# Optimization experiments

Measured on AMD Instinct MI355X. Metric: run time of the kernel, lower is better.

The kernel has to match this reference:

```python
import jax, jax.numpy as jnp
import numpy as np

NF = 32
B, H, W = 4, 256, 256


def conv(x, w, b, pad):
    y = jax.lax.conv_general_dilated(x, w, (1, 1), [(pad, pad), (pad, pad)],
                                     dimension_numbers=('NCHW', 'OIHW', 'NCHW'))
    return y + b[None, :, None, None]


def maxpool(x):  # kernel 3, stride 2, pad 1 (pad with -inf like torch)
    return jax.lax.reduce_window(x, -jnp.inf, jax.lax.max,
                                 (1, 1, 3, 3), (1, 1, 2, 2),
                                 [(0, 0), (0, 0), (1, 1), (1, 1)])


def up2(x):  # bilinear x2, align_corners=False (half-pixel) == jax.image default
    b, c, h, w = x.shape
    return jax.image.resize(x, (b, c, 2 * h, 2 * w), 'bilinear')


def norm_gates(g1, g2, g3):
    s = jnp.abs(g1) + jnp.abs(g2) + jnp.abs(g3)
    s = jnp.where(s == 0, 1e-6, s)
    m = (s >= 1).astype(g1.dtype)
    return tuple((1 - m) * g + m * (g / s) for g in (g1, g2, g3))


def propagate(x, g1, g2, g3, horizontal, reverse):
    """GateRecurrent2dnoind: sequential gated scan along one spatial axis.
    h[t] = (1 - g1 - g2 - g3) * x[t] + g1*h[t-1](i-1) + g2*h[t-1](i) + g3*h[t-1](i+1)
    with zero boundary for out-of-range neighbors."""
    if not horizontal:
        x, g1, g2, g3 = (jnp.swapaxes(t, 2, 3) for t in (x, g1, g2, g3))
    if reverse:
        x, g1, g2, g3 = (t[..., ::-1] for t in (x, g1, g2, g3))
    seqs = tuple(jnp.moveaxis(t, 3, 0) for t in (x, g1, g2, g3))  # [W,B,C,H]

    def step(h, inp):
        xt, a1, a2, a3 = inp
        z = jnp.zeros_like(h[..., :1])
        h_up = jnp.concatenate([z, h[..., :-1]], axis=-1)   # neighbor i-1
        h_dn = jnp.concatenate([h[..., 1:], z], axis=-1)    # neighbor i+1
        hn = (1 - a1 - a2 - a3) * xt + a1 * h_up + a2 * h + a3 * h_dn
        return hn, hn

    h0 = jnp.zeros(x.shape[:3], x.dtype)
    _, ys = jax.lax.scan(step, h0, seqs)
    out = jnp.moveaxis(ys, 0, 3)
    if reverse:
        out = out[..., ::-1]
    if not horizontal:
        out = jnp.swapaxes(out, 2, 3)
    return out


def spn_forward(x, rgb, mw, mb, c1w, c1b, c2w, c2b, c3w, c3b, c4w, c4b,
                d0w, d0b, d2w, d2b, d4w, d4b, d6w, d6b, d7w, d7b, pw, pb):
    nf = NF
    X = conv(x, mw, mb, 1)
    # VGG encoder
    f1 = conv(rgb, c1w, c1b, 1)
    p = maxpool(jax.nn.relu(f1))
    f2 = conv(p, c2w, c2b, 1)
    p = maxpool(jax.nn.relu(f2))
    f3 = conv(p, c3w, c3b, 1)
    p3 = maxpool(jax.nn.relu(f3))
    f4 = conv(p3, c4w, c4b, 1)
    # Decoder
    o = conv(f4, d0w, d0b, 0)
    o = jax.nn.elu(conv(up2(o), d2w, d2b, 1)) + f3
    o = jax.nn.elu(conv(up2(o), d4w, d4b, 1)) + f2
    o = jax.nn.elu(conv(up2(o), d6w, d6b, 1)) + f1
    guide = conv(o, d7w, d7b, 1)  # [B, 12*nf, H, W]
    G = [guide[:, i * nf:(i + 1) * nf] for i in range(12)]
    dirs = [(True, False), (True, True), (False, False), (False, True)]
    outs = []
    for k, (hor, rev) in enumerate(dirs):
        g1, g2, g3 = norm_gates(G[3 * k], G[3 * k + 1], G[3 * k + 2])
        outs.append(propagate(X, g1, g2, g3, hor, rev))
    out = jnp.maximum(jnp.maximum(outs[0], outs[1]), jnp.maximum(outs[2], outs[3]))
    return conv(out, pw, pb, 1)


def setup_inputs() -> dict:
    key = jax.random.key(0)
    ks = jax.random.split(key, 32)
    nf = NF

    def p(k, shape):
        return jax.random.normal(k, shape, dtype=jnp.float32) * 0.1

    inp = {
        'x': jax.random.normal(ks[0], (B, 3, H, W), dtype=jnp.float32),
        'rgb': jax.random.normal(ks[1], (B, 3, H, W), dtype=jnp.float32),
        'mw': p(ks[2], (nf, 3, 3, 3)), 'mb': p(ks[3], (nf,)),
        'c1w': p(ks[4], (nf, 3, 3, 3)), 'c1b': p(ks[5], (nf,)),
        'c2w': p(ks[6], (nf * 2, nf, 3, 3)), 'c2b': p(ks[7], (nf * 2,)),
        'c3w': p(ks[8], (nf * 4, nf * 2, 3, 3)), 'c3b': p(ks[9], (nf * 4,)),
        'c4w': p(ks[10], (nf * 8, nf * 4, 3, 3)), 'c4b': p(ks[11], (nf * 8,)),
        'd0w': p(ks[12], (nf * 4, nf * 8, 1, 1)), 'd0b': p(ks[13], (nf * 4,)),
        'd2w': p(ks[14], (nf * 4, nf * 4, 3, 3)), 'd2b': p(ks[15], (nf * 4,)),
        'd4w': p(ks[16], (nf * 2, nf * 4, 3, 3)), 'd4b': p(ks[17], (nf * 2,)),
        'd6w': p(ks[18], (nf, nf * 2, 3, 3)), 'd6b': p(ks[19], (nf,)),
        'd7w': p(ks[20], (nf * 12, nf, 3, 3)), 'd7b': p(ks[21], (nf * 12,)),
        'pw': p(ks[22], (3, nf, 3, 3)), 'pb': p(ks[23], (3,)),
    }
    return inp


def reference(x, rgb, mw, mb, c1w, c1b, c2w, c2b, c3w, c3b, c4w, c4b,
              d0w, d0b, d2w, d2b, d4w, d4b, d6w, d6b, d7w, d7b, pw, pb):
    return spn_forward(x, rgb, mw, mb, c1w, c1b, c2w, c2b, c3w, c3b, c4w, c4b,
                       d0w, d0b, d2w, d2b, d4w, d4b, d6w, d6b, d7w, d7b, pw, pb)
```

## Files before the change

### kernel.cpp

```cpp
#include <hip/hip_runtime.h>
#include <cstddef>
#include <cstdint>

#define DEVINL __device__ __forceinline__

typedef __attribute__((ext_vector_type(8))) _Float16 half8v;
typedef __attribute__((ext_vector_type(4))) _Float16 half4v;
typedef __attribute__((ext_vector_type(16))) float f32x16;

constexpr int cmax(int a, int b) { return a > b ? a : b; }


__global__ __launch_bounds__(256) void k_repack(
    const float* __restrict__ src, float* __restrict__ dst, int Cin, int Cout)
{
  int n = Cout * Cin * 9;
  int e = blockIdx.x * 256 + threadIdx.x;
  if (e >= n) return;
  int co = e / (Cin * 9);
  int r  = e - co * Cin * 9;
  int ci = r / 9;
  int k  = r - ci * 9;
  dst[(ci * 9 + k) * Cout + co] = src[e];
}

__global__ __launch_bounds__(256) void k_packwh(
    const float* __restrict__ src, _Float16* __restrict__ dst, int Cin, int Cout)
{
  int chunks = Cin >> 4;
  int total = Cout * chunks * 144;
  int e = blockIdx.x * 256 + threadIdx.x;
  if (e >= total) return;
  int n  = e / (chunks * 144);
  int r2 = e - n * chunks * 144;
  int cb = r2 / 144;
  int k  = r2 - cb * 144;
  int tap = k >> 4, ci = k & 15;
  float v = src[((size_t)n * Cin + cb * 16 + ci) * 9 + tap];
  dst[((size_t)cb * Cout + n) * 152 + k] = (_Float16)v;
}

template<int NWM, int NACC, int CHUNKS, int MODE, int GATES>
__global__ __launch_bounds__(NWM * 64) void k_convh(
    const float* __restrict__ in, const _Float16* __restrict__ wpk,
    const float* __restrict__ bias, const float* __restrict__ skip,
    void* __restrict__ outv,
    int H, int W, int wCout, int n0, int outC, int oco0)
{
  static_assert(GATES == 0 || NACC == 3, "GATES needs NACC==3");
  constexpr int NTHR = NWM * 64;
  constexpr int ROWS = NWM * 2;
  constexpr int RH = ROWS + 2;
  constexpr int N_BLK = NACC * 32;
  constexpr int MT = NWM * 32;
  constexpr int A_BYTES = RH * 18 * 16 * 2;
  constexpr int B_BYTES = N_BLK * 152 * 2;
  constexpr int MPF = MT + 1;
  constexpr int MPH = 132;
  constexpr int EP_BYTES = GATES ? (96 * MPH * 2) : (N_BLK * MPF * 4);
  constexpr int SMEM = cmax(A_BYTES + B_BYTES, EP_BYTES);

  const int tid = threadIdx.x;
  const int wave = tid >> 6, lane = tid & 63;
  const int wm = wave;
  const int tiles_x = W >> 4;
  const int tx0 = (blockIdx.x % tiles_x) << 4;
  const int ty0 = (blockIdx.x / tiles_x) * ROWS;
  const int b = blockIdx.z;
  const int nb = n0 + blockIdx.y * N_BLK;
  const int ocb = oco0 + blockIdx.y * N_BLK;

  __shared__ __align__(16) char smem[SMEM];
  _Float16* Ah = (_Float16*)smem;
  _Float16* Bh = (_Float16*)(smem + A_BYTES);

  f32x16 acc[NACC] = {};

  const size_t ps = (size_t)H * W;
  const float* inb = in + (size_t)b * (CHUNKS * 16) * ps;

  for (int cb = 0; cb < CHUNKS; ++cb) {
    __syncthreads();
    for (int e = tid; e < RH * 18; e += NTHR) {
      int r = e / 18, c = e - r * 18;
      int gy = ty0 + r - 1, gx = tx0 + c - 1;
      bool ok = (unsigned)gy < (unsigned)H && (unsigned)gx < (unsigned)W;
      const float* src = inb + (size_t)(cb * 16) * ps + (size_t)gy * W + gx;
      half8v v0, v1;
#pragma unroll
      for (int j = 0; j < 8; ++j)
        v0[j] = ok ? (_Float16)src[(size_t)j * ps] : (_Float16)0.f;
#pragma unroll
      for (int j = 0; j < 8; ++j)
        v1[j] = ok ? (_Float16)src[(size_t)(j + 8) * ps] : (_Float16)0.f;
      *(half8v*)&Ah[e * 16] = v0;
      *(half8v*)&Ah[e * 16 + 8] = v1;
    }
    {
      const _Float16* wsrc = wpk + ((size_t)cb * wCout + nb) * 152;
      for (int e = tid; e < N_BLK * 19; e += NTHR)
        *(uint4*)&Bh[e * 8] = *(const uint4*)(wsrc + e * 8);
    }
    __syncthreads();
    const int am = wm * 32 + (lane & 31);
    const int r0 = am >> 4, c0 = am & 15;
    const int kh = lane >> 5;
    const _Float16* Ab = Ah + kh * 8;
    const _Float16* Bb = Bh + kh * 8;
#pragma unroll
    for (int ks = 0; ks < 9; ++ks) {
      const int dy = ks / 3, dx = ks - dy * 3;
      half8v af = *(const half8v*)(Ab + ((r0 + dy) * 18 + (c0 + dx)) * 16);
#pragma unroll
      for (int na = 0; na < NACC; ++na) {
        const int bn = na * 32 + (lane & 31);
        half8v bf = *(const half8v*)(Bb + bn * 152 + ks * 16);
        acc[na] = __builtin_amdgcn_mfma_f32_32x32x16_f16(af, bf, acc[na], 0, 0, 0);
      }
    }
  }

  __syncthreads();

  if (GATES) {
    _Float16* EPH = (_Float16*)smem;
    const int c = lane & 31;
    const float bv0 = bias[nb + c];
    const float bv1 = bias[nb + 32 + c];
    const float bv2 = bias[nb + 64 + c];
#pragma unroll
    for (int i = 0; i < 16; ++i) {
      int m = wm * 32 + (i & 3) + 8 * (i >> 2) + 4 * (lane >> 5);
      float g1 = acc[0][i] + bv0;
      float g2 = acc[GATES ? 1 : 0][i] + bv1;
      float g3 = acc[GATES ? 2 : 0][i] + bv2;
      float s = fabsf(g1) + fabsf(g2) + fabsf(g3);
      if (s >= 1.f) { float r = 1.f / s; g1 *= r; g2 *= r; g3 *= r; }
      EPH[(size_t)(0 * 32 + c) * MPH + m] = (_Float16)g1;
      EPH[(size_t)(1 * 32 + c) * MPH + m] = (_Float16)g2;
      EPH[(size_t)(2 * 32 + c) * MPH + m] = (_Float16)g3;
    }
    __syncthreads();
    _Float16* outh = (_Float16*)outv;
    if (MODE == 2) {
      const int TOT = 96 * 16;
      for (int r = tid; r < TOT; r += NTHR) {
        int gc = r >> 4, x = r & 15;
        const _Float16* ep = EPH + (size_t)gc * MPH + x;
        _Float16 v[8];
#pragma unroll
        for (int y = 0; y < 8; ++y) v[y] = ep[y * 16];
        size_t base = ((size_t)(b * 96 + gc) * W + tx0 + x) * (size_t)H + ty0;
        *(uint4*)(outh + base) = *(const uint4*)v;
      }
    } else {
      const int TOT = 96 * ROWS;
      for (int r = tid; r < TOT; r += NTHR) {
        int gc = r / ROWS, y = r - gc * ROWS;
        const _Float16* ep = EPH + (size_t)gc * MPH + y * 16;
        _Float16 v[16];
#pragma unroll
        for (int x = 0; x < 16; ++x) v[x] = ep[x];
        size_t base = ((size_t)(b * 96 + gc) * H + ty0 + y) * (size_t)W + tx0;
        *(uint4*)(outh + base) = *(const uint4*)v;
        *(uint4*)(outh + base + 8) = *(const uint4*)(v + 8);
      }
    }
  } else {
    float* EP = (float*)smem;
    float bv[NACC];
#pragma unroll
    for (int na = 0; na < NACC; ++na) bv[na] = bias[nb + na * 32 + (lane & 31)];
#pragma unroll
    for (int na = 0; na < NACC; ++na) {
      const int c = na * 32 + (lane & 31);
#pragma unroll
      for (int i = 0; i < 16; ++i) {
        int m = wm * 32 + (i & 3) + 8 * (i >> 2) + 4 * (lane >> 5);
        EP[(size_t)c * MPF + m] = acc[na][i] + bv[na];
      }
    }
    __syncthreads();
    float* out = (float*)outv;
    const int TOT = N_BLK * ROWS;
    for (int r = tid; r < TOT; r += NTHR) {
      int c = r / ROWS, y = r - c * ROWS;
      const float* ep = EP + (size_t)c * MPF + y * 16;
      float v[16];
#pragma unroll
      for (int x = 0; x < 16; ++x) v[x] = ep[x];
      size_t base = (((size_t)b * outC + ocb + c) * H + ty0 + y) * (size_t)W + tx0;
      if (MODE == 1) {
#pragma unroll
        for (int j = 0; j < 4; ++j) {
          float4 sk = *(const float4*)(skip + base + 4 * j);
          float e0 = v[4*j+0] > 0.f ? v[4*j+0] : expm1f(v[4*j+0]);
          float e1 = v[4*j+1] > 0.f ? v[4*j+1] : expm1f(v[4*j+1]);
          float e2 = v[4*j+2] > 0.f ? v[4*j+2] : expm1f(v[4*j+2]);
          float e3 = v[4*j+3] > 0.f ? v[4*j+3] : expm1f(v[4*j+3]);
          v[4*j+0] = e0 + sk.x; v[4*j+1] = e1 + sk.y;
          v[4*j+2] = e2 + sk.z; v[4*j+3] = e3 + sk.w;
        }
      }
#pragma unroll
      for (int j = 0; j < 4; ++j)
        *(float4*)(out + base + 4 * j) = *(const float4*)(v + 4 * j);
    }
  }
}

template<int CI, int CO>
__global__ __launch_bounds__(256) void k_conv3x3f(
    const float* __restrict__ in, const float* __restrict__ wr,
    const float* __restrict__ bias, float* __restrict__ out,
    int Cin, int H, int W, int wstride, int outC)
{
  const int ntx = W >> 4;
  const int tid = threadIdx.x;
  const int tx = tid & 15, ty = tid >> 4;
  const int tx0 = (blockIdx.x % ntx) << 4, ty0 = (blockIdx.x / ntx) << 4;
  const int b = blockIdx.z;

  __shared__ float sh[CI * 324];

  float acc[CO];
#pragma unroll
  for (int co = 0; co < CO; ++co) acc[co] = bias[co];

  const float* inb = in + (size_t)b * Cin * H * W;

  for (int cb = 0; cb < Cin; cb += CI) {
    __syncthreads();
    for (int e = tid; e < CI * 324; e += 256) {
      int ci = e / 324;
      int rr = e - ci * 324;
      int r = rr / 18, c = rr - r * 18;
      int gh = ty0 + r - 1, gw = tx0 + c - 1;
      float v = 0.f;
      if ((unsigned)gh < (unsigned)H && (unsigned)gw < (unsigned)W)
        v = inb[(size_t)(cb + ci) * H * W + (size_t)gh * W + gw];
      sh[e] = v;
    }
    __syncthreads();
#pragma unroll 1
    for (int ci = 0; ci < CI; ++ci) {
      float v[9];
      const float* sp = sh + ci * 324 + ty * 18 + tx;
#pragma unroll
      for (int kh = 0; kh < 3; ++kh)
#pragma unroll
        for (int kw = 0; kw < 3; ++kw)
          v[kh * 3 + kw] = sp[kh * 18 + kw];
      const float* wp = wr + (size_t)((cb + ci) * 9) * wstride;
#pragma unroll
      for (int k = 0; k < 9; ++k)
#pragma unroll
        for (int co = 0; co < CO; ++co)
          acc[co] = fmaf(wp[(size_t)k * wstride + co], v[k], acc[co]);
    }
  }
#pragma unroll
  for (int co = 0; co < CO; ++co)
    out[(((size_t)b * outC + co) * H + ty0 + ty) * W + tx0 + tx] = acc[co];
}

__global__ __launch_bounds__(256) void k_convfin(
    const _Float16* __restrict__ om1, const _Float16* __restrict__ om2,
    const _Float16* __restrict__ omT1, const _Float16* __restrict__ omT2,
    const float* __restrict__ wr, const float* __restrict__ bias,
    float* __restrict__ out)
{
  const int H = 256, W = 256;
  const int tid = threadIdx.x;
  const int tx = tid & 15, ty = tid >> 4;
  const int tx0 = (blockIdx.x & 15) << 4, ty0 = (blockIdx.x >> 4) << 4;
  const int b = blockIdx.z;

  __shared__ float sh[32 * 324];

  for (int e = tid; e < 32 * 324; e += 256) {
    int ci = e / 324, rr = e - ci * 324;
    int r = rr / 18, c = rr - r * 18;
    int gh = ty0 + r - 1, gw = tx0 + c - 1;
    float v = 0.f;
    if ((unsigned)gh < (unsigned)H && (unsigned)gw < (unsigned)W) {
      size_t p = ((size_t)(b * 32 + ci) * H + gh) * W + gw;
      v = fmaxf((float)om1[p], (float)om2[p]);
    }
    sh[ci * 324 + r * 18 + c] = v;
  }
  __syncthreads();
  for (int e = tid; e < 32 * 324; e += 256) {
    int ci = e / 324, rr = e - ci * 324;
    int c = rr / 18, r = rr - c * 18;
    int gh = ty0 + r - 1, gw = tx0 + c - 1;
    if ((unsigned)gh < (unsigned)H && (unsigned)gw < (unsigned)W) {
      size_t p = ((size_t)(b * 32 + ci) * W + gw) * (size_t)H + gh;
      float t = fmaxf((float)omT1[p], (float)omT2[p]);
      int si = ci * 324 + r * 18 + c;
      sh[si] = fmaxf(sh[si], t);
    }
  }
  __syncthreads();

  float acc[3] = {bias[0], bias[1], bias[2]};
#pragma unroll 1
  for (int ci = 0; ci < 32; ++ci) {
    float v[9];
    const float* sp = sh + ci * 324 + ty * 18 + tx;
#pragma unroll
    for (int kh = 0; kh < 3; ++kh)
#pragma unroll
      for (int kw = 0; kw < 3; ++kw)
        v[kh * 3 + kw] = sp[kh * 18 + kw];
    const float* wp = wr + (size_t)(ci * 9) * 3;
#pragma unroll
    for (int k = 0; k < 9; ++k)
#pragma unroll
      for (int co = 0; co < 3; ++co)
        acc[co] = fmaf(wp[(size_t)k * 3 + co], v[k], acc[co]);
  }
#pragma unroll
  for (int co = 0; co < 3; ++co)
    out[(((size_t)b * 3 + co) * H + ty0 + ty) * W + tx0 + tx] = acc[co];
}

__global__ __launch_bounds__(256) void k_conv1x1(
    const float* __restrict__ in, const float* __restrict__ wgt,
    const float* __restrict__ bias, float* __restrict__ out,
    int Cin, int Cout, int H, int W)
{
  int hw = blockIdx.x * 256 + threadIdx.x;
  if (hw >= H * W) return;
  int co = blockIdx.y, b = blockIdx.z;
  const float* ip = in + (size_t)b * Cin * H * W + hw;
  const float* wp = wgt + (size_t)co * Cin;
  float acc = bias[co];
  for (int ci = 0; ci < Cin; ++ci) acc += wp[ci] * ip[(size_t)ci * H * W];
  out[((size_t)b * Cout + co) * H * W + hw] = acc;
}

__global__ __launch_bounds__(256) void k_pool(
    const float* __restrict__ in, float* __restrict__ out, int C, int H, int W)
{
  int Ho = H >> 1, Wo = W >> 1;
  int hw = blockIdx.x * 256 + threadIdx.x;
  if (hw >= Ho * Wo) return;
  int ow = hw % Wo, oh = hw / Wo;
  int c = blockIdx.y, b = blockIdx.z;
  const float* p = in + ((size_t)(b * C + c) * H) * W;
  float m = 0.f;
#pragma unroll
  for (int dh = -1; dh <= 1; ++dh) {
    int ih = 2 * oh + dh;
    if ((unsigned)ih >= (unsigned)H) continue;
    const float* r = p + (size_t)ih * W;
#pragma unroll
    for (int dw = -1; dw <= 1; ++dw) {
      int iw = 2 * ow + dw;
      if ((unsigned)iw >= (unsigned)W) continue;
      m = fmaxf(m, r[iw]);
    }
  }
  out[((size_t)(b * C + c) * Ho + oh) * Wo + ow] = m;
}

__global__ __launch_bounds__(256) void k_up2(
    const float* __restrict__ in, float* __restrict__ out, int C, int H, int W)
{
  int Ho = H * 2, Wo = W * 2;
  int hw = blockIdx.x * 256 + threadIdx.x;
  if (hw >= Ho * Wo) return;
  int ow = hw % Wo, oh = hw / Wo;
  int c = blockIdx.y, b = blockIdx.z;
  int ih = oh >> 1, iw = ow >> 1;
  int ih0, ih1, iw0, iw1; float fh0, fw0;
  if (oh & 1) { ih0 = ih; ih1 = min(ih + 1, H - 1); fh0 = 0.75f; }
  else        { ih0 = max(ih - 1, 0); ih1 = ih;     fh0 = 0.25f; }
  if (ow & 1) { iw0 = iw; iw1 = min(iw + 1, W - 1); fw0 = 0.75f; }
  else        { iw0 = max(iw - 1, 0); iw1 = iw;     fw0 = 0.25f; }
  const float* p = in + ((size_t)(b * C + c) * H) * W;
  float v = fh0 * (fw0 * p[(size_t)ih0 * W + iw0] + (1.f - fw0) * p[(size_t)ih0 * W + iw1])
          + (1.f - fh0) * (fw0 * p[(size_t)ih1 * W + iw0] + (1.f - fw0) * p[(size_t)ih1 * W + iw1]);
  out[((size_t)(b * C + c) * Ho + oh) * Wo + ow] = v;
}

__global__ void k_xcvt(const float* __restrict__ in, _Float16* __restrict__ xn,
                       _Float16* __restrict__ xt)
{
  __shared__ _Float16 t[32][33];
  int z = blockIdx.z;
  int x0 = blockIdx.x * 32, y0 = blockIdx.y * 32;
  int tx = threadIdx.x, ty = threadIdx.y;
  const float* ip = in + (size_t)z * 65536;
#pragma unroll
  for (int j = 0; j < 32; j += 8) {
    float v = ip[(size_t)(y0 + ty + j) * 256 + x0 + tx];
    xn[(size_t)z * 65536 + (size_t)(y0 + ty + j) * 256 + x0 + tx] = (_Float16)v;
    t[ty + j][tx] = (_Float16)v;
  }
  __syncthreads();
#pragma unroll
  for (int j = 0; j < 32; j += 8)
    xt[(size_t)z * 65536 + (size_t)(x0 + ty + j) * 256 + y0 + tx] = t[tx][ty + j];
}

DEVINL void gl_lds16p(const void* g, void* lds) {
  __builtin_amdgcn_global_load_lds(
      (const __attribute__((address_space(1))) unsigned int*)g,
      (__attribute__((address_space(3))) unsigned int*)lds, 16, 0, 0);
}

template<int REV>
DEVINL void prop_core(const _Float16* xp, const _Float16* g1,
                      const _Float16* g2, const _Float16* g3,
                      _Float16* op, int S, int P, int lane,
                      _Float16* bx, _Float16* h1, _Float16* h2, _Float16* h3)
{
  float r0 = 0.f, r1 = 0.f, r2 = 0.f, r3 = 0.f;
  int cur = 0;

  auto stage = [&](int buf, int s0) {
#pragma unroll
    for (int v = 0; v < 8; ++v) {
      size_t ro = (size_t)(s0 + 2 * v) * P + lane * 8;
      gl_lds16p(xp + ro, bx + buf * 4096 + v * 512);
      gl_lds16p(g1 + ro, h1 + buf * 4096 + v * 512);
      gl_lds16p(g2 + ro, h2 + buf * 4096 + v * 512);
      gl_lds16p(g3 + ro, h3 + buf * 4096 + v * 512);
    }
  };

  stage(0, REV ? (S - 16) : 0);
  const int NT = S / 16;
  for (int t = 0; t < NT; ++t) {
    const int s0 = REV ? (S - 16 - t * 16) : (t * 16);
    asm volatile("s_waitcnt vmcnt(0)" ::: "memory");
    if (t + 1 < NT) stage(cur ^ 1, REV ? (s0 - 16) : (s0 + 16));

#pragma unroll
    for (int u = 0; u < 16; ++u) {
      const int e = REV ? (15 - u) : u;
      half4v xv = *(const half4v*)(bx + cur * 4096 + e * 256 + 4 * lane);
      half4v a1 = *(const half4v*)(h1 + cur * 4096 + e * 256 + 4 * lane);
      half4v a2 = *(const half4v*)(h2 + cur * 4096 + e * 256 + 4 * lane);
      half4v a3 = *(const half4v*)(h3 + cur * 4096 + e * 256 + 4 * lane);

      float hu0 = __shfl_up(r3, 1);
      float hd3 = __shfl_down(r0, 1);
      if (lane == 0)  hu0 = 0.f;
      if (lane == 63) hd3 = 0.f;

      float o0 = r0, o1 = r1, o2 = r2, o3v = r3;
      float x0 = xv[0], x1 = xv[1], x2 = xv[2], x3 = xv[3];
      float a10 = a1[0], a11 = a1[1], a12 = a1[2], a13 = a1[3];
      float a20 = a2[0], a21 = a2[1], a22 = a2[2], a23 = a2[3];
      float a30 = a3[0], a31 = a3[1], a32 = a3[2], a33 = a3[3];

      r0 = (1.f - a10 - a20 - a30) * x0 + a10 * hu0 + a20 * o0 + a30 * o1;
      r1 = (1.f - a11 - a21 - a31) * x1 + a11 * o0  + a21 * o1 + a31 * o2;
      r2 = (1.f - a12 - a22 - a32) * x2 + a12 * o1  + a22 * o2 + a32 * o3v;
      r3 = (1.f - a13 - a23 - a33) * x3 + a13 * o2  + a23 * o3v + a33 * hd3;

      half4v hv; hv[0] = (_Float16)r0; hv[1] = (_Float16)r1;
      hv[2] = (_Float16)r2; hv[3] = (_Float16)r3;
      *(half4v*)(op + (size_t)(s0 + e) * P + 4 * lane) = hv;
    }
    cur ^= 1;
  }
}

__global__ __launch_bounds__(64) void k_prop_pair(
    const _Float16* __restrict__ Xh,
    const _Float16* __restrict__ GA, const _Float16* __restrict__ GB,
    _Float16* __restrict__ omA, _Float16* __restrict__ omB, int S, int P)
{
  const int dir = blockIdx.x >> 7;
  const int plane = blockIdx.x & 127;
  const int b = plane >> 5, c = plane & 31;
  const int lane = threadIdx.x;
  const size_t ps = (size_t)S * P;

  __shared__ __align__(16) _Float16 bx[2 * 4096];
  __shared__ __align__(16) _Float16 h1[2 * 4096];
  __shared__ __align__(16) _Float16 h2[2 * 4096];
  __shared__ __align__(16) _Float16 h3[2 * 4096];

  const _Float16* xp = Xh + (size_t)plane * ps;
  const _Float16* G = dir ? GB : GA;
  const _Float16* g1 = G + ((size_t)b * 96 + c) * ps;
  const _Float16* g2 = g1 + (size_t)32 * ps;
  const _Float16* g3 = g1 + (size_t)64 * ps;
  _Float16* op = (dir ? omB : omA) + (size_t)plane * ps;

  if (dir == 0) prop_core<0>(xp, g1, g2, g3, op, S, P, lane, bx, h1, h2, h3);
  else          prop_core<1>(xp, g1, g2, g3, op, S, P, lane, bx, h1, h2, h3);
}

extern "C" void kernel_launch(void* const* d_in, const int* in_sizes, int n_in,
                              void* d_out, int out_size, void* d_ws, size_t ws_size,
                              hipStream_t stream)
{
  const float* x   = (const float*)d_in[0];
  const float* rgb = (const float*)d_in[1];
  const float* mw  = (const float*)d_in[2];
  const float* mb  = (const float*)d_in[3];
  const float* c1w = (const float*)d_in[4];
  const float* c1b = (const float*)d_in[5];
  const float* c2w = (const float*)d_in[6];
  const float* c2b = (const float*)d_in[7];
  const float* c3w = (const float*)d_in[8];
  const float* c3b = (const float*)d_in[9];
  const float* c4w = (const float*)d_in[10];
  const float* c4b = (const float*)d_in[11];
  const float* d0w = (const float*)d_in[12];
  const float* d0b = (const float*)d_in[13];
  const float* d2w = (const float*)d_in[14];
  const float* d2b = (const float*)d_in[15];
  const float* d4w = (const float*)d_in[16];
  const float* d4b = (const float*)d_in[17];
  const float* d6w = (const float*)d_in[18];
  const float* d6b = (const float*)d_in[19];
  const float* d7w = (const float*)d_in[20];
  const float* d7b = (const float*)d_in[21];
  const float* pw  = (const float*)d_in[22];
  const float* pb  = (const float*)d_in[23];

  char* ws = (char*)d_ws;
  const size_t MB = 1024 * 1024;
  _Float16* Xn16 = (_Float16*)(ws + 0);
  _Float16* Xt16 = (_Float16*)(ws + 16 * MB);
  float* X32f = (float*)(ws + 32 * MB);
  float* f1   = (float*)(ws + 64 * MB);
  float* f2   = (float*)(ws + 96 * MB);
  float* f3   = (float*)(ws + 112 * MB);
  float* p1   = (float*)(ws + 120 * MB);
  float* p2   = (float*)(ws + 128 * MB);
  float* p3   = (float*)(ws + 132 * MB);
  float* f4   = (float*)(ws + 134 * MB);
  float* o0   = (float*)(ws + 138 * MB);
  float* u0   = (float*)(ws + 140 * MB);
  float* o1   = (float*)(ws + 148 * MB);
  float* u1   = (float*)(ws + 32 * MB);
  float* o2   = (float*)(ws + 160 * MB);
  float* u2   = (float*)(ws + 96 * MB);
  float* o3   = (float*)(ws + 160 * MB);
  _Float16* gbufA = (_Float16*)(ws + 32 * MB);
  _Float16* gbufB = (_Float16*)(ws + 80 * MB);
  _Float16* om1  = (_Float16*)(ws + 128 * MB);
  _Float16* om2  = (_Float16*)(ws + 144 * MB);
  _Float16* omT1 = (_Float16*)(ws + 0);
  _Float16* omT2 = (_Float16*)(ws + 160 * MB);
  char* wz = ws + 192 * MB;
  float* wmf  = (float*)wz;
  float* wc1f = wmf + 864;
  float* wpkf = wc1f + 864;
  _Float16* wc2p = (_Float16*)(wpkf + 864);
  _Float16* wc3p = wc2p + 19456;
  _Float16* wc4p = wc3p + 77824;
  _Float16* wd2p = wc4p + 311296;
  _Float16* wd4p = wd2p + 155648;
  _Float16* wd6p = wd4p + 77824;
  _Float16* wd7p = wd6p + 19456;

  hipMemsetAsync(d_ws, 0, 194 * MB, stream);

  dim3 blk(256);
  auto repf = [&](const float* s, float* d, int ci, int co) {
    int n = co * ci * 9;
    k_repack<<<dim3((n + 255) / 256), blk, 0, stream>>>(s, d, ci, co);
  };
  auto packh = [&](const float* s, _Float16* d, int ci, int co) {
    int n = co * (ci / 16) * 144;
    k_packwh<<<dim3((n + 255) / 256), blk, 0, stream>>>(s, d, ci, co);
  };
  repf(mw, wmf, 3, 32);
  repf(c1w, wc1f, 3, 32);
  repf(pw, wpkf, 32, 3);
  packh(c2w, wc2p, 32, 64);
  packh(c3w, wc3p, 64, 128);
  packh(c4w, wc4p, 128, 256);
  packh(d2w, wd2p, 128, 128);
  packh(d4w, wd4p, 128, 64);
  packh(d6w, wd6p, 64, 32);
  packh(d7w, wd7p, 32, 384);

  k_conv3x3f<3, 32><<<dim3(256, 1, 4), blk, 0, stream>>>(x, wmf, mb, X32f, 3, 256, 256, 32, 32);
  k_xcvt<<<dim3(8, 8, 128), dim3(32, 8), 0, stream>>>(X32f, Xn16, Xt16);
  k_conv3x3f<3, 32><<<dim3(256, 1, 4), blk, 0, stream>>>(rgb, wc1f, c1b, f1, 3, 256, 256, 32, 32);

  k_pool<<<dim3(64, 32, 4), blk, 0, stream>>>(f1, p1, 32, 256, 256);
  k_convh<4, 2, 2, 0, 0><<<dim3(128, 1, 4), dim3(256), 0, stream>>>(p1, wc2p, c2b, nullptr, f2, 128, 128, 64, 0, 64, 0);
  k_pool<<<dim3(16, 64, 4), blk, 0, stream>>>(f2, p2, 64, 128, 128);
  k_convh<2, 2, 4, 0, 0><<<dim3(64, 2, 4), dim3(128), 0, stream>>>(p2, wc3p, c3b, nullptr, f3, 64, 64, 128, 0, 128, 0);
  k_pool<<<dim3(4, 128, 4), blk, 0, stream>>>(f3, p3, 128, 64, 64);
  k_convh<2, 2, 8, 0, 0><<<dim3(16, 4, 4), dim3(128), 0, stream>>>(p3, wc4p, c4b, nullptr, f4, 32, 32, 256, 0, 256, 0);
  k_conv1x1<<<dim3(4, 128, 4), blk, 0, stream>>>(f4, d0w, d0b, o0, 256, 128, 32, 32);

  k_up2<<<dim3(16, 128, 4), blk, 0, stream>>>(o0, u0, 128, 32, 32);
  k_convh<2, 2, 8, 1, 0><<<dim3(64, 2, 4), dim3(128), 0, stream>>>(u0, wd2p, d2b, f3, o1, 64, 64, 128, 0, 128, 0);
  k_up2<<<dim3(64, 128, 4), blk, 0, stream>>>(o1, u1, 128, 64, 64);
  k_convh<4, 2, 8, 1, 0><<<dim3(128, 1, 4), dim3(256), 0, stream>>>(u1, wd4p, d4b, f2, o2, 128, 128, 64, 0, 64, 0);
  k_up2<<<dim3(256, 64, 4), blk, 0, stream>>>(o2, u2, 64, 128, 128);
  k_convh<4, 1, 4, 1, 0><<<dim3(512, 1, 4), dim3(256), 0, stream>>>(u2, wd6p, d6b, f1, o3, 256, 256, 32, 0, 32, 0);

  k_convh<4, 3, 2, 0, 1><<<dim3(512, 1, 4), dim3(256), 0, stream>>>(o3, wd7p, d7b, nullptr, gbufA, 256, 256, 384, 192, 96, 0);
  k_convh<4, 3, 2, 0, 1><<<dim3(512, 1, 4), dim3(256), 0, stream>>>(o3, wd7p, d7b, nullptr, gbufB, 256, 256, 384, 288, 96, 0);
  k_prop_pair<<<dim3(256), dim3(64), 0, stream>>>(Xn16, gbufA, gbufB, om1, om2, 256, 256);

  k_convh<4, 3, 2, 2, 1><<<dim3(512, 1, 4), dim3(256), 0, stream>>>(o3, wd7p, d7b, nullptr, gbufA, 256, 256, 384, 0, 96, 0);
  k_convh<4, 3, 2, 2, 1><<<dim3(512, 1, 4), dim3(256), 0, stream>>>(o3, wd7p, d7b, nullptr, gbufB, 256, 256, 384, 96, 96, 0);
  k_prop_pair<<<dim3(256), dim3(64), 0, stream>>>(Xt16, gbufA, gbufB, omT1, omT2, 256, 256);

  k_convfin<<<dim3(256, 1, 4), blk, 0, stream>>>(om1, om2, omT1, omT2, wpkf, pb, (float*)d_out);
}
```

Baseline: 934.9 us.

## Merge paired gate-conv launches and split final conv into transpose-max plus conv

Each pair of gate-producing conv launches becomes one launch with a grid y-dimension of 2, and blockIdx.y picks the output buffer. The fused final kernel, which read the transposed propagation outputs with strided gathers, is replaced by two kernels. The first takes the max of the four outputs and transposes through a padded shared-memory tile so that global accesses are coalesced. The second runs the generic 3x3 conv over the resulting fp32 buffer. This aims to remove uncoalesced loads and one launch per pair, but adds a full fp32 intermediate write and read.

```diff
diff --git a/kernel.cpp b/kernel.cpp
--- a/kernel.cpp
+++ b/kernel.cpp
@@ -44,7 +44,7 @@
 __global__ __launch_bounds__(NWM * 64) void k_convh(
     const float* __restrict__ in, const _Float16* __restrict__ wpk,
     const float* __restrict__ bias, const float* __restrict__ skip,
-    void* __restrict__ outv,
+    void* __restrict__ outv, void* __restrict__ outv2,
     int H, int W, int wCout, int n0, int outC, int oco0)
 {
   static_assert(GATES == 0 || NACC == 3, "GATES needs NACC==3");
@@ -141,7 +141,7 @@
       EPH[(size_t)(2 * 32 + c) * MPH + m] = (_Float16)g3;
     }
     __syncthreads();
-    _Float16* outh = (_Float16*)outv;
+    _Float16* outh = (_Float16*)(blockIdx.y ? outv2 : outv);
     if (MODE == 2) {
       const int TOT = 96 * 16;
       for (int r = tid; r < TOT; r += NTHR) {
@@ -264,65 +264,29 @@
     out[(((size_t)b * outC + co) * H + ty0 + ty) * W + tx0 + tx] = acc[co];
 }
 
-__global__ __launch_bounds__(256) void k_convfin(
+__global__ __launch_bounds__(256) void k_max4(
     const _Float16* __restrict__ om1, const _Float16* __restrict__ om2,
     const _Float16* __restrict__ omT1, const _Float16* __restrict__ omT2,
-    const float* __restrict__ wr, const float* __restrict__ bias,
     float* __restrict__ out)
 {
-  const int H = 256, W = 256;
-  const int tid = threadIdx.x;
-  const int tx = tid & 15, ty = tid >> 4;
-  const int tx0 = (blockIdx.x & 15) << 4, ty0 = (blockIdx.x >> 4) << 4;
-  const int b = blockIdx.z;
-
-  __shared__ float sh[32 * 324];
-
-  for (int e = tid; e < 32 * 324; e += 256) {
-    int ci = e / 324, rr = e - ci * 324;
-    int r = rr / 18, c = rr - r * 18;
-    int gh = ty0 + r - 1, gw = tx0 + c - 1;
-    float v = 0.f;
-    if ((unsigned)gh < (unsigned)H && (unsigned)gw < (unsigned)W) {
-      size_t p = ((size_t)(b * 32 + ci) * H + gh) * W + gw;
-      v = fmaxf((float)om1[p], (float)om2[p]);
-    }
-    sh[ci * 324 + r * 18 + c] = v;
+  __shared__ float t[32][33];
+  const int z = blockIdx.z;
+  const int x0 = blockIdx.x * 32, y0 = blockIdx.y * 32;
+  const int tx = threadIdx.x & 31, ty = threadIdx.x >> 5;
+  const size_t ps = 65536;
+  const size_t zb = (size_t)z * ps;
+#pragma unroll
+  for (int j = 0; j < 32; j += 8) {
+    size_t p = zb + (size_t)(x0 + ty + j) * 256 + (y0 + tx);
+    t[ty + j][tx] = fmaxf((float)omT1[p], (float)omT2[p]);
   }
   __syncthreads();
-  for (int e = tid; e < 32 * 324; e += 256) {
-    int ci = e / 324, rr = e - ci * 324;
-    int c = rr / 18, r = rr - c * 18;
-    int gh = ty0 + r - 1, gw = tx0 + c - 1;
-    if ((unsigned)gh < (unsigned)H && (unsigned)gw < (unsigned)W) {
-      size_t p = ((size_t)(b * 32 + ci) * W + gw) * (size_t)H + gh;
-      float t = fmaxf((float)omT1[p], (float)omT2[p]);
-      int si = ci * 324 + r * 18 + c;
-      sh[si] = fmaxf(sh[si], t);
-    }
-  }
-  __syncthreads();
-
-  float acc[3] = {bias[0], bias[1], bias[2]};
-#pragma unroll 1
-  for (int ci = 0; ci < 32; ++ci) {
-    float v[9];
-    const float* sp = sh + ci * 324 + ty * 18 + tx;
-#pragma unroll
-    for (int kh = 0; kh < 3; ++kh)
-#pragma unroll
-      for (int kw = 0; kw < 3; ++kw)
-        v[kh * 3 + kw] = sp[kh * 18 + kw];
-    const float* wp = wr + (size_t)(ci * 9) * 3;
-#pragma unroll
-    for (int k = 0; k < 9; ++k)
-#pragma unroll
-      for (int co = 0; co < 3; ++co)
-        acc[co] = fmaf(wp[(size_t)k * 3 + co], v[k], acc[co]);
-  }
-#pragma unroll
-  for (int co = 0; co < 3; ++co)
-    out[(((size_t)b * 3 + co) * H + ty0 + ty) * W + tx0 + tx] = acc[co];
+#pragma unroll
+  for (int j = 0; j < 32; j += 8) {
+    size_t p = zb + (size_t)(y0 + ty + j) * 256 + (x0 + tx);
+    float v = fmaxf((float)om1[p], (float)om2[p]);
+    out[p] = fmaxf(v, t[tx][ty + j]);
+  }
 }
 
 __global__ __launch_bounds__(256) void k_conv1x1(
@@ -551,6 +515,7 @@
   _Float16* om2  = (_Float16*)(ws + 144 * MB);
   _Float16* omT1 = (_Float16*)(ws + 0);
   _Float16* omT2 = (_Float16*)(ws + 160 * MB);
+  float* omfin = (float*)(ws + 32 * MB);
   char* wz = ws + 192 * MB;
   float* wmf  = (float*)wz;
   float* wc1f = wmf + 864;
@@ -590,27 +555,26 @@
   k_conv3x3f<3, 32><<<dim3(256, 1, 4), blk, 0, stream>>>(rgb, wc1f, c1b, f1, 3, 256, 256, 32, 32);
 
   k_pool<<<dim3(64, 32, 4), blk, 0, stream>>>(f1, p1, 32, 256, 256);
-  k_convh<4, 2, 2, 0, 0><<<dim3(128, 1, 4), dim3(256), 0, stream>>>(p1, wc2p, c2b, nullptr, f2, 128, 128, 64, 0, 64, 0);
+  k_convh<4, 2, 2, 0, 0><<<dim3(128, 1, 4), dim3(256), 0, stream>>>(p1, wc2p, c2b, nullptr, f2, nullptr, 128, 128, 64, 0, 64, 0);
   k_pool<<<dim3(16, 64, 4), blk, 0, stream>>>(f2, p2, 64, 128, 128);
-  k_convh<2, 2, 4, 0, 0><<<dim3(64, 2, 4), dim3(128), 0, stream>>>(p2, wc3p, c3b, nullptr, f3, 64, 64, 128, 0, 128, 0);
+  k_convh<2, 2, 4, 0, 0><<<dim3(64, 2, 4), dim3(128), 0, stream>>>(p2, wc3p, c3b, nullptr, f3, nullptr, 64, 64, 128, 0, 128, 0);
   k_pool<<<dim3(4, 128, 4), blk, 0, stream>>>(f3, p3, 128, 64, 64);
-  k_convh<2, 2, 8, 0, 0><<<dim3(16, 4, 4), dim3(128), 0, stream>>>(p3, wc4p, c4b, nullptr, f4, 32, 32, 256, 0, 256, 0);
+  k_convh<2, 2, 8, 0, 0><<<dim3(16, 4, 4), dim3(128), 0, stream>>>(p3, wc4p, c4b, nullptr, f4, nullptr, 32, 32, 256, 0, 256, 0);
   k_conv1x1<<<dim3(4, 128, 4), blk, 0, stream>>>(f4, d0w, d0b, o0, 256, 128, 32, 32);
 
   k_up2<<<dim3(16, 128, 4), blk, 0, stream>>>(o0, u0, 128, 32, 32);
-  k_convh<2, 2, 8, 1, 0><<<dim3(64, 2, 4), dim3(128), 0, stream>>>(u0, wd2p, d2b, f3, o1, 64, 64, 128, 0, 128, 0);
+  k_convh<2, 2, 8, 1, 0><<<dim3(64, 2, 4), dim3(128), 0, stream>>>(u0, wd2p, d2b, f3, o1, nullptr, 64, 64, 128, 0, 128, 0);
   k_up2<<<dim3(64, 128, 4), blk, 0, stream>>>(o1, u1, 128, 64, 64);
-  k_convh<4, 2, 8, 1, 0><<<dim3(128, 1, 4), dim3(256), 0, stream>>>(u1, wd4p, d4b, f2, o2, 128, 128, 64, 0, 64, 0);
+  k_convh<4, 2, 8, 1, 0><<<dim3(128, 1, 4), dim3(256), 0, stream>>>(u1, wd4p, d4b, f2, o2, nullptr, 128, 128, 64, 0, 64, 0);
   k_up2<<<dim3(256, 64, 4), blk, 0, stream>>>(o2, u2, 64, 128, 128);
-  k_convh<4, 1, 4, 1, 0><<<dim3(512, 1, 4), dim3(256), 0, stream>>>(u2, wd6p, d6b, f1, o3, 256, 256, 32, 0, 32, 0);
-
-  k_convh<4, 3, 2, 0, 1><<<dim3(512, 1, 4), dim3(256), 0, stream>>>(o3, wd7p, d7b, nullptr, gbufA, 256, 256, 384, 192, 96, 0);
-  k_convh<4, 3, 2, 0, 1><<<dim3(512, 1, 4), dim3(256), 0, stream>>>(o3, wd7p, d7b, nullptr, gbufB, 256, 256, 384, 288, 96, 0);
+  k_convh<4, 1, 4, 1, 0><<<dim3(512, 1, 4), dim3(256), 0, stream>>>(u2, wd6p, d6b, f1, o3, nullptr, 256, 256, 32, 0, 32, 0);
+
+  k_convh<4, 3, 2, 0, 1><<<dim3(512, 2, 4), dim3(256), 0, stream>>>(o3, wd7p, d7b, nullptr, gbufA, gbufB, 256, 256, 384, 192, 96, 0);
   k_prop_pair<<<dim3(256), dim3(64), 0, stream>>>(Xn16, gbufA, gbufB, om1, om2, 256, 256);
 
-  k_convh<4, 3, 2, 2, 1><<<dim3(512, 1, 4), dim3(256), 0, stream>>>(o3, wd7p, d7b, nullptr, gbufA, 256, 256, 384, 0, 96, 0);
-  k_convh<4, 3, 2, 2, 1><<<dim3(512, 1, 4), dim3(256), 0, stream>>>(o3, wd7p, d7b, nullptr, gbufB, 256, 256, 384, 96, 96, 0);
+  k_convh<4, 3, 2, 2, 1><<<dim3(512, 2, 4), dim3(256), 0, stream>>>(o3, wd7p, d7b, nullptr, gbufA, gbufB, 256, 256, 384, 0, 96, 0);
   k_prop_pair<<<dim3(256), dim3(64), 0, stream>>>(Xt16, gbufA, gbufB, omT1, omT2, 256, 256);
 
-  k_convfin<<<dim3(256, 1, 4), blk, 0, stream>>>(om1, om2, omT1, omT2, wpkf, pb, (float*)d_out);
-}
+  k_max4<<<dim3(8, 8, 128), blk, 0, stream>>>(om1, om2, omT1, omT2, omfin);
+  k_conv3x3f<32, 3><<<dim3(256, 1, 4), blk, 0, stream>>>(omfin, wpkf, pb, (float*)d_out, 32, 256, 256, 3, 3);
+}
```

Result: faster. 915.8 us (-2.0%).
